# Kernel optimization log

Measured on AMD Instinct MI355X. Metric: run time of the kernel, lower is better.

Reference implementation:

```python
import jax, jax.numpy as jnp
import numpy as np

B, S, D_IN, D_OUT = 4, 4096, 512, 64

def setup_inputs() -> dict:
    key = jax.random.key(0)
    k1, k2, k3, k4, k5, k6 = jax.random.split(key, 6)
    return {
        "key_inputs": jax.random.normal(k1, (B, S, D_IN), dtype=jnp.float32),
        "value_inputs": jax.random.normal(k2, (B, S, D_IN), dtype=jnp.float32),
        "query_inputs": jax.random.normal(k3, (B, S, D_IN), dtype=jnp.float32),
        "Wk": jax.random.normal(k4, (D_IN, D_OUT), dtype=jnp.float32) * 0.02,
        "Wv": jax.random.normal(k5, (D_IN, D_OUT), dtype=jnp.float32) * 0.02,
        "Wq": jax.random.normal(k6, (D_IN, D_OUT), dtype=jnp.float32) * 0.02,
    }

def reference(key_inputs, value_inputs, query_inputs, Wk, Wv, Wq):
    # projections: [B,S,D_in] @ [D_in,D_out] -> [B,S,D_out]
    K = jnp.einsum('bsd,de->bse', key_inputs, Wk)
    V = jnp.einsum('bsd,de->bse', value_inputs, Wv)
    Q = jnp.einsum('bsd,de->bse', query_inputs, Wq)
    d = K.shape[2]
    scores = jnp.einsum('bqe,bke->bqk', Q, K)  # [B,S,S]
    # strictly upper-triangular -inf causal mask (added BEFORE scaling, as in source)
    causal = jnp.triu(jnp.ones((scores.shape[1], scores.shape[2]), dtype=bool), k=1)
    scores = jnp.where(causal[None], -jnp.inf, scores)
    attn = jax.nn.softmax(scores / jnp.sqrt(jnp.float32(d)), axis=-1)
    Z = jnp.einsum('bqk,bke->bqe', attn, V)  # [B,S,D_out]
    return Z
```

## Files before the change

### kernel.cpp

```cpp
#include <hip/hip_runtime.h>
#include <hip/hip_bf16.h>

#define B_ 4
#define S_ 4096
#define DIN 512
#define DOUT 64
#define QB 64
#define KVB 64
#define NCHUNK_TOT 288

typedef __attribute__((ext_vector_type(8))) short short8;
typedef __attribute__((ext_vector_type(4))) float f32x4;

static __device__ __forceinline__ float fast_exp2(float x) {
    return __builtin_amdgcn_exp2f(x);
}

static __device__ __forceinline__ unsigned short f2bf(float x) {
    union { float f; unsigned u; } v; v.f = x;
    unsigned r = v.u + 0x7FFF + ((v.u >> 16) & 1);
    return (unsigned short)(r >> 16);
}

static __device__ __forceinline__ unsigned bf2pack(float a, float b) {
    __hip_bfloat162 h = __float22bfloat162_rn({a, b});
    return *reinterpret_cast<unsigned*>(&h);
}

static __device__ __forceinline__ void gload_lds16(const void* g, void* l) {
    __builtin_amdgcn_global_load_lds(
        (const __attribute__((address_space(1))) void*)g,
        (__attribute__((address_space(3))) void*)l, 16, 0, 0);
}

__global__ __launch_bounds__(256) void wt_kernel(
    const float* __restrict__ Wq, const float* __restrict__ Wk,
    const float* __restrict__ Wv, unsigned short* __restrict__ wt)
{
    __shared__ float tile[64 * 65];
    int p = blockIdx.y;
    int k0 = blockIdx.x * 64;
    const float* w = (p == 0) ? Wq : ((p == 1) ? Wk : Wv);
    unsigned short* o = wt + (size_t)p * DIN * DOUT;
    int t = threadIdx.x;
    for (int i = 0; i < 16; ++i) {
        int flat = i * 256 + t;
        int ki = flat >> 6, di = flat & 63;
        tile[ki * 65 + di] = w[(size_t)(k0 + ki) * DOUT + di];
    }
    __syncthreads();
    for (int i = 0; i < 16; ++i) {
        int flat = i * 256 + t;
        int d = flat >> 6, k = flat & 63;
        o[(size_t)d * DIN + k0 + k] = f2bf(tile[k * 65 + d]);
    }
}

__global__ __launch_bounds__(256) void proj_kernel(
    const float* __restrict__ q_in, const float* __restrict__ k_in,
    const float* __restrict__ v_in, const unsigned short* __restrict__ wt,
    unsigned short* __restrict__ qb, unsigned short* __restrict__ kb,
    unsigned short* __restrict__ vtb)
{
    __shared__ float a_lds[2][64 * 64];
    __shared__ unsigned short b_lds[2][64 * 64];
    int p = blockIdx.y;
    const float* in = (p == 0) ? q_in : ((p == 1) ? k_in : v_in);
    const unsigned short* w = wt + (size_t)p * DIN * DOUT;
    int tid = threadIdx.x, wv = tid >> 6, lane = tid & 63;
    int lrow = lane & 15, lkhi = lane >> 4;
    int m0 = blockIdx.x * 64;
    int m0w = m0 + wv * 16;

    const char* in_b = (const char*)(in + (size_t)m0 * DIN);
    const char* w_b  = (const char*)w;

#define PSTAGE(buf, kc_) do {                                                   \
    _Pragma("unroll")                                                           \
    for (int i = 0; i < 4; ++i) {                                 \
        int drow = i * 16 + wv * 4 + (lane >> 4);                               \
        int offg = ((lane & 15) * 16) ^ ((drow & 7) << 5);                      \
        const char* g = in_b + (size_t)drow * 2048 + (kc_) * 256 + offg;        \
        gload_lds16(g, (char*)a_lds[buf] + i * 4096 + wv * 1024);               \
    }                                                                           \
    _Pragma("unroll")                                                           \
    for (int i = 0; i < 2; ++i) {                                  \
        int drow = i * 32 + wv * 8 + (lane >> 3);                               \
        int offg = ((lane & 7) * 16) ^ ((drow & 7) << 4);                       \
        const char* g = w_b + (size_t)drow * 1024 + (kc_) * 128 + offg;         \
        gload_lds16(g, (char*)b_lds[buf] + i * 4096 + wv * 1024);               \
    }                                                                           \
} while (0)

    PSTAGE(0, 0);
    asm volatile("s_waitcnt vmcnt(0)" ::: "memory");
    __builtin_amdgcn_s_barrier();
    asm volatile("" ::: "memory");

    f32x4 acc[4] = {};
    int row_a = wv * 16 + lrow;
    int abase = row_a * 256;
    int axor = (row_a & 7) << 5;
    int cur = 0;

#pragma unroll
    for (int kc = 0; kc < 8; ++kc) {
        if (kc < 7) {
            PSTAGE(cur ^ 1, kc + 1);
            asm volatile("s_waitcnt vmcnt(6)" ::: "memory");
        } else {
            asm volatile("s_waitcnt vmcnt(0)" ::: "memory");
        }
        __builtin_amdgcn_s_barrier();
        asm volatile("" ::: "memory");

        const char* abuf = (const char*)a_lds[cur];
        const char* bbuf = (const char*)b_lds[cur];
#pragma unroll
        for (int kk = 0; kk < 2; ++kk) {
            int aoff = abase + ((kk * 128 + lkhi * 32) ^ axor);
            float4 x0 = *reinterpret_cast<const float4*>(abuf + aoff);
            float4 x1 = *reinterpret_cast<const float4*>(abuf + aoff + 16);
            short8 af;
            unsigned* au = reinterpret_cast<unsigned*>(&af);
            au[0] = bf2pack(x0.x, x0.y);
            au[1] = bf2pack(x0.z, x0.w);
            au[2] = bf2pack(x1.x, x1.y);
            au[3] = bf2pack(x1.z, x1.w);
#pragma unroll
            for (int ct = 0; ct < 4; ++ct) {
                int row_b = ct * 16 + lrow;
                int boff = row_b * 128 + ((kk * 64 + lkhi * 16) ^ ((row_b & 7) << 4));
                short8 bf = *reinterpret_cast<const short8*>(bbuf + boff);
                acc[ct] = __builtin_amdgcn_mfma_f32_16x16x32_bf16(af, bf, acc[ct], 0, 0, 0);
            }
        }
        __builtin_amdgcn_s_barrier();
        asm volatile("" ::: "memory");
        cur ^= 1;
    }
#undef PSTAGE

    float scale = (p == 0) ? 0.18033688011112042f : 1.0f;
    for (int ct = 0; ct < 4; ++ct) {
        for (int r = 0; r < 4; ++r) {
            int row = m0w + lkhi * 4 + r;
            int col = ct * 16 + lrow;
            unsigned short val = f2bf(acc[ct][r] * scale);
            if (p == 0)       qb[(size_t)row * DOUT + col] = val;
            else if (p == 1)  kb[(size_t)row * DOUT + col] = val;
            else {
                int bb = row >> 12, ss = row & 4095;
                vtb[((size_t)bb * DOUT + col) * S_ + ss] = val;
            }
        }
    }
}

__global__ __launch_bounds__(256) void attn_part(
    const unsigned short* __restrict__ qb, const unsigned short* __restrict__ kb,
    const unsigned short* __restrict__ vtb, float* __restrict__ Opart,
    float* __restrict__ ml)
{
    __shared__ unsigned short k_lds[2][KVB * DOUT];
    __shared__ unsigned short v_lds[2][DOUT * KVB];
    __shared__ unsigned short p_lds[4][16 * KVB];

    int b = blockIdx.y;
    int x = NCHUNK_TOT - 1 - blockIdx.x;
    int m = 0;
    while (4 * (m + 1) * (m + 2) <= x) ++m;
    int rem = x - 4 * m * (m + 1);
    int j = rem / (m + 1), c = rem % (m + 1);
    int qt = 8 * m + j;

    int q0 = qt * QB;
    int tid = threadIdx.x, wv = tid >> 6, lane = tid & 63;
    int lrow = lane & 15, lkhi = lane >> 4;
    int lkhi4 = lkhi * 4;
    int qloc = wv * 16 + lrow;

    const unsigned short* Qbase = qb + ((size_t)b * S_ + q0 + wv * 16 + lrow) * DOUT;
    short8 qf[2];
    qf[0] = *reinterpret_cast<const short8*>(Qbase + lkhi * 8);
    qf[1] = *reinterpret_cast<const short8*>(Qbase + 32 + lkhi * 8);

    f32x4 o[4] = {};
    float m_run = -INFINITY, l_run = 0.f;

    const unsigned short* Kg = kb + (size_t)b * S_ * DOUT;
    const unsigned short* Vg = vtb + (size_t)b * DOUT * S_;
    char* pw = reinterpret_cast<char*>(p_lds[wv]);

    int srow_lo = (lane >> 3);
    int schunk = (lane & 7) * 16;
    int soff = schunk ^ (srow_lo << 4);

    int kv_beg = c * 8;
    int kv_end = min(kv_beg + 8, qt + 1);
    int cur = 0;

#define STAGE(buf, kvt_) do {                                                  \
    int kv0_ = (kvt_) * KVB;                                                   \
    for (int h = 0; h < 2; ++h) {                                              \
        int r_ = wv * 16 + h * 8 + srow_lo;                                    \
        const char* gk_ = (const char*)(Kg + (size_t)(kv0_ + r_) * DOUT) + soff; \
        gload_lds16(gk_, (char*)k_lds[buf] + wv * 2048 + h * 1024);            \
        const char* gv_ = (const char*)(Vg + (size_t)r_ * S_ + kv0_) + soff;   \
        gload_lds16(gv_, (char*)v_lds[buf] + wv * 2048 + h * 1024);            \
    }                                                                          \
} while (0)

    STAGE(0, kv_beg);
    asm volatile("s_waitcnt vmcnt(0)" ::: "memory");
    __builtin_amdgcn_s_barrier();
    asm volatile("" ::: "memory");

    for (int kvt = kv_beg; kvt < kv_end; ++kvt) {
        if (kvt + 1 < kv_end) STAGE(cur ^ 1, kvt + 1);

        const char* kl = (const char*)k_lds[cur];
        const char* vl = (const char*)v_lds[cur];

        f32x4 sc[4];
        __builtin_amdgcn_s_setprio(1);
        for (int ct = 0; ct < 4; ++ct) {
            f32x4 a = {};
            for (int ds = 0; ds < 2; ++ds) {
                int r = ct * 16 + lrow;
                int byte = (r * 128 + (ds * 32 + lkhi * 8) * 2) ^ ((r & 7) << 4);
                short8 kf = *reinterpret_cast<const short8*>(kl + byte);
                a = __builtin_amdgcn_mfma_f32_16x16x32_bf16(kf, qf[ds], a, 0, 0, 0);
            }
            sc[ct] = a;
        }
        __builtin_amdgcn_s_setprio(0);

        if (kvt == qt) {
            for (int ct = 0; ct < 4; ++ct)
                for (int r = 0; r < 4; ++r)
                    if (ct * 16 + lkhi4 + r > qloc) sc[ct][r] = -INFINITY;
        }

        float mx4[4];
        for (int ct = 0; ct < 4; ++ct)
            mx4[ct] = fmaxf(fmaxf(sc[ct][0], sc[ct][1]), fmaxf(sc[ct][2], sc[ct][3]));
        float mxl = fmaxf(fmaxf(mx4[0], mx4[1]), fmaxf(mx4[2], mx4[3]));
        mxl = fmaxf(mxl, __shfl_xor(mxl, 16));
        mxl = fmaxf(mxl, __shfl_xor(mxl, 32));
        float mnew = fmaxf(m_run, mxl);
        float corr = fast_exp2(m_run - mnew);

        float s4[4];
        for (int ct = 0; ct < 4; ++ct) {
            sc[ct][0] = fast_exp2(sc[ct][0] - mnew);
            sc[ct][1] = fast_exp2(sc[ct][1] - mnew);
            sc[ct][2] = fast_exp2(sc[ct][2] - mnew);
            sc[ct][3] = fast_exp2(sc[ct][3] - mnew);
            s4[ct] = (sc[ct][0] + sc[ct][1]) + (sc[ct][2] + sc[ct][3]);
        }
        float rs = (s4[0] + s4[1]) + (s4[2] + s4[3]);
        rs += __shfl_xor(rs, 16);
        rs += __shfl_xor(rs, 32);
        l_run = l_run * corr + rs;
        m_run = mnew;

        float corrq[4];
        for (int r = 0; r < 4; ++r) corrq[r] = __shfl(corr, lkhi4 + r);
        for (int ct2 = 0; ct2 < 4; ++ct2)
            for (int r = 0; r < 4; ++r)
                o[ct2][r] *= corrq[r];

        for (int ct = 0; ct < 4; ++ct) {
            uint2 pk;
            pk.x = bf2pack(sc[ct][0], sc[ct][1]);
            pk.y = bf2pack(sc[ct][2], sc[ct][3]);
            int byte = (lrow * 128 + (ct * 16 + lkhi4) * 2) ^ ((lrow & 7) << 4);
            *reinterpret_cast<uint2*>(pw + byte) = pk;
        }

        __builtin_amdgcn_s_setprio(1);
        for (int ct2 = 0; ct2 < 4; ++ct2) {
            for (int ks = 0; ks < 2; ++ks) {
                int pbyte = (lrow * 128 + (ks * 32 + lkhi * 8) * 2) ^ ((lrow & 7) << 4);
                short8 pf = *reinterpret_cast<const short8*>(pw + pbyte);
                int vr = ct2 * 16 + lrow;
                int vbyte = (vr * 128 + (ks * 32 + lkhi * 8) * 2) ^ ((vr & 7) << 4);
                short8 vf = *reinterpret_cast<const short8*>(vl + vbyte);
                o[ct2] = __builtin_amdgcn_mfma_f32_16x16x32_bf16(pf, vf, o[ct2], 0, 0, 0);
            }
        }
        __builtin_amdgcn_s_setprio(0);
        __syncthreads();
        cur ^= 1;
    }
#undef STAGE

    float* Op = Opart + ((size_t)b * NCHUNK_TOT + x) * (64 * 64);
    float* Ml = ml + ((size_t)b * NCHUNK_TOT + x) * (64 * 2);
    for (int r = 0; r < 4; ++r) {
        int qr = wv * 16 + lkhi4 + r;
        for (int ct2 = 0; ct2 < 4; ++ct2)
            Op[qr * 64 + ct2 * 16 + lrow] = o[ct2][r];
    }
    if (lkhi == 0) {
        int qr = wv * 16 + lrow;
        Ml[qr * 2 + 0] = m_run;
        Ml[qr * 2 + 1] = l_run;
    }
}

__global__ __launch_bounds__(256) void attn_combine(
    const float* __restrict__ Opart, const float* __restrict__ ml,
    float* __restrict__ out)
{
    int qt = blockIdx.x, b = blockIdx.y;
    int m = qt >> 3;
    int nch = m + 1;
    int cbase = 4 * m * (m + 1) + (qt - 8 * m) * nch;

    int r = threadIdx.x >> 2;
    int cg = (threadIdx.x & 3) * 16;

    float M = -INFINITY;
    for (int c = 0; c < nch; ++c)
        M = fmaxf(M, ml[(((size_t)b * NCHUNK_TOT + cbase + c) * 64 + r) * 2]);

    float L = 0.f;
    f32x4 acc[4] = {};
    for (int c = 0; c < nch; ++c) {
        size_t ci = (size_t)b * NCHUNK_TOT + cbase + c;
        float mc = ml[(ci * 64 + r) * 2 + 0];
        float lc = ml[(ci * 64 + r) * 2 + 1];
        float w = fast_exp2(mc - M);
        L += lc * w;
        const f32x4* Op = reinterpret_cast<const f32x4*>(Opart + ci * (64 * 64) + r * 64 + cg);
        for (int i = 0; i < 4; ++i) {
            f32x4 v = Op[i];
            acc[i] += v * w;
        }
    }
    float inv = 1.f / L;
    f32x4* dst = reinterpret_cast<f32x4*>(out + (((size_t)b * S_) + qt * 64 + r) * DOUT + cg);
    for (int i = 0; i < 4; ++i)
        dst[i] = acc[i] * inv;
}

extern "C" void kernel_launch(void* const* d_in, const int* in_sizes, int n_in,
                              void* d_out, int out_size, void* d_ws, size_t ws_size,
                              hipStream_t stream) {
    const float* key_in = (const float*)d_in[0];
    const float* val_in = (const float*)d_in[1];
    const float* qry_in = (const float*)d_in[2];
    const float* Wk = (const float*)d_in[3];
    const float* Wv = (const float*)d_in[4];
    const float* Wq = (const float*)d_in[5];
    float* out = (float*)d_out;

    char* ws = (char*)d_ws;
    size_t off = 0;
    unsigned short* qb  = (unsigned short*)(ws + off); off += (size_t)B_ * S_ * DOUT * 2;
    unsigned short* kb  = (unsigned short*)(ws + off); off += (size_t)B_ * S_ * DOUT * 2;
    unsigned short* vtb = (unsigned short*)(ws + off); off += (size_t)B_ * S_ * DOUT * 2;
    unsigned short* wt  = (unsigned short*)(ws + off); off += (size_t)3 * DIN * DOUT * 2;
    float* Opart = (float*)(ws + off); off += (size_t)B_ * NCHUNK_TOT * 64 * 64 * 4;
    float* ml    = (float*)(ws + off); off += (size_t)B_ * NCHUNK_TOT * 64 * 2 * 4;

    wt_kernel<<<dim3(8, 3), 256, 0, stream>>>(Wq, Wk, Wv, wt);
    proj_kernel<<<dim3(256, 3), 256, 0, stream>>>(qry_in, key_in, val_in, wt, qb, kb, vtb);
    attn_part<<<dim3(NCHUNK_TOT, B_), 256, 0, stream>>>(qb, kb, vtb, Opart, ml);
    attn_combine<<<dim3(S_ / QB, B_), 256, 0, stream>>>(Opart, ml, out);
}
```

Before: 63.97 us.

## Split projection into fp32-to-bf16 conversion pass and bf16 GEMM kernel

Adds a separate streaming kernel that converts the fp32 Q/K/V inputs to bf16 into a scratch buffer aliased onto the partial-output workspace. The projection GEMM then loads bf16 tiles directly into LDS, halving its A-tile LDS footprint and dropping the in-loop conversion. In exchange the inputs are read in fp32, written back in bf16 and read again, which adds global memory traffic and an extra kernel launch on a bandwidth-bound stage.

```diff
diff --git a/kernel.cpp b/kernel.cpp
--- a/kernel.cpp
+++ b/kernel.cpp
@@ -56,39 +56,50 @@
     }
 }
 
-__global__ __launch_bounds__(256) void proj_kernel(
+__global__ __launch_bounds__(256) void conv_kernel(
     const float* __restrict__ q_in, const float* __restrict__ k_in,
-    const float* __restrict__ v_in, const unsigned short* __restrict__ wt,
+    const float* __restrict__ v_in, unsigned short* __restrict__ abf)
+{
+    int p = blockIdx.y;
+    const float* in = (p == 0) ? q_in : ((p == 1) ? k_in : v_in);
+    unsigned short* o = abf + (size_t)p * B_ * S_ * DIN;
+    size_t n8 = (size_t)B_ * S_ * DIN / 8;
+    size_t stride = (size_t)gridDim.x * blockDim.x;
+    for (size_t i = (size_t)blockIdx.x * blockDim.x + threadIdx.x; i < n8; i += stride) {
+        const float4* src = reinterpret_cast<const float4*>(in + i * 8);
+        float4 x0 = src[0], x1 = src[1];
+        short8 v;
+        unsigned* u = reinterpret_cast<unsigned*>(&v);
+        u[0] = bf2pack(x0.x, x0.y); u[1] = bf2pack(x0.z, x0.w);
+        u[2] = bf2pack(x1.x, x1.y); u[3] = bf2pack(x1.z, x1.w);
+        *reinterpret_cast<short8*>(o + i * 8) = v;
+    }
+}
+
+__global__ __launch_bounds__(256) void gemm_kernel(
+    const unsigned short* __restrict__ abf, const unsigned short* __restrict__ wt,
     unsigned short* __restrict__ qb, unsigned short* __restrict__ kb,
     unsigned short* __restrict__ vtb)
 {
-    __shared__ float a_lds[2][64 * 64];
+    __shared__ unsigned short a_lds[2][64 * 64];
     __shared__ unsigned short b_lds[2][64 * 64];
     int p = blockIdx.y;
-    const float* in = (p == 0) ? q_in : ((p == 1) ? k_in : v_in);
-    const unsigned short* w = wt + (size_t)p * DIN * DOUT;
+    const char* a_g = (const char*)(abf + (size_t)p * B_ * S_ * DIN
+                                        + (size_t)blockIdx.x * 64 * DIN);
+    const char* w_g = (const char*)(wt + (size_t)p * DIN * DOUT);
     int tid = threadIdx.x, wv = tid >> 6, lane = tid & 63;
     int lrow = lane & 15, lkhi = lane >> 4;
-    int m0 = blockIdx.x * 64;
-    int m0w = m0 + wv * 16;
-
-    const char* in_b = (const char*)(in + (size_t)m0 * DIN);
-    const char* w_b  = (const char*)w;
+    int m0w = blockIdx.x * 64 + wv * 16;
 
 #define PSTAGE(buf, kc_) do {                                                   \
     _Pragma("unroll")                                                           \
-    for (int i = 0; i < 4; ++i) {                                 \
-        int drow = i * 16 + wv * 4 + (lane >> 4);                               \
-        int offg = ((lane & 15) * 16) ^ ((drow & 7) << 5);                      \
-        const char* g = in_b + (size_t)drow * 2048 + (kc_) * 256 + offg;        \
-        gload_lds16(g, (char*)a_lds[buf] + i * 4096 + wv * 1024);               \
-    }                                                                           \
-    _Pragma("unroll")                                                           \
-    for (int i = 0; i < 2; ++i) {                                  \
-        int drow = i * 32 + wv * 8 + (lane >> 3);                               \
+    for (int h = 0; h < 2; ++h) {                                               \
+        int drow = h * 32 + wv * 8 + (lane >> 3);                               \
         int offg = ((lane & 7) * 16) ^ ((drow & 7) << 4);                       \
-        const char* g = w_b + (size_t)drow * 1024 + (kc_) * 128 + offg;         \
-        gload_lds16(g, (char*)b_lds[buf] + i * 4096 + wv * 1024);               \
+        gload_lds16(a_g + (size_t)drow * 1024 + (kc_) * 128 + offg,             \
+                    (char*)a_lds[buf] + h * 4096 + wv * 1024);                  \
+        gload_lds16(w_g + (size_t)drow * 1024 + (kc_) * 128 + offg,             \
+                    (char*)b_lds[buf] + h * 4096 + wv * 1024);                  \
     }                                                                           \
 } while (0)
 
@@ -99,15 +110,14 @@
 
     f32x4 acc[4] = {};
     int row_a = wv * 16 + lrow;
-    int abase = row_a * 256;
-    int axor = (row_a & 7) << 5;
+    int axor = (row_a & 7) << 4;
     int cur = 0;
 
 #pragma unroll
     for (int kc = 0; kc < 8; ++kc) {
         if (kc < 7) {
             PSTAGE(cur ^ 1, kc + 1);
-            asm volatile("s_waitcnt vmcnt(6)" ::: "memory");
+            asm volatile("s_waitcnt vmcnt(4)" ::: "memory");
         } else {
             asm volatile("s_waitcnt vmcnt(0)" ::: "memory");
         }
@@ -118,15 +128,8 @@
         const char* bbuf = (const char*)b_lds[cur];
 #pragma unroll
         for (int kk = 0; kk < 2; ++kk) {
-            int aoff = abase + ((kk * 128 + lkhi * 32) ^ axor);
-            float4 x0 = *reinterpret_cast<const float4*>(abuf + aoff);
-            float4 x1 = *reinterpret_cast<const float4*>(abuf + aoff + 16);
-            short8 af;
-            unsigned* au = reinterpret_cast<unsigned*>(&af);
-            au[0] = bf2pack(x0.x, x0.y);
-            au[1] = bf2pack(x0.z, x0.w);
-            au[2] = bf2pack(x1.x, x1.y);
-            au[3] = bf2pack(x1.z, x1.w);
+            int aoff = row_a * 128 + ((kk * 64 + lkhi * 16) ^ axor);
+            short8 af = *reinterpret_cast<const short8*>(abuf + aoff);
 #pragma unroll
             for (int ct = 0; ct < 4; ++ct) {
                 int row_b = ct * 16 + lrow;
@@ -365,9 +368,11 @@
     unsigned short* wt  = (unsigned short*)(ws + off); off += (size_t)3 * DIN * DOUT * 2;
     float* Opart = (float*)(ws + off); off += (size_t)B_ * NCHUNK_TOT * 64 * 64 * 4;
     float* ml    = (float*)(ws + off); off += (size_t)B_ * NCHUNK_TOT * 64 * 2 * 4;
+    unsigned short* abf = (unsigned short*)Opart;
 
     wt_kernel<<<dim3(8, 3), 256, 0, stream>>>(Wq, Wk, Wv, wt);
-    proj_kernel<<<dim3(256, 3), 256, 0, stream>>>(qry_in, key_in, val_in, wt, qb, kb, vtb);
+    conv_kernel<<<dim3(1024, 3), 256, 0, stream>>>(qry_in, key_in, val_in, abf);
+    gemm_kernel<<<dim3(256, 3), 256, 0, stream>>>(abf, wt, qb, kb, vtb);
     attn_part<<<dim3(NCHUNK_TOT, B_), 256, 0, stream>>>(qb, kb, vtb, Opart, ml);
     attn_combine<<<dim3(S_ / QB, B_), 256, 0, stream>>>(Opart, ml, out);
 }
```

New measurement: 79.39 us. 24.1% more time.
